# Kernel optimization log

Hardware: AMD Instinct MI355X
Metric: run time of the kernel (lower is better)

## Reference

```python
import jax, jax.numpy as jnp
import numpy as np

B, S, E, H, L, VL, VOCAB = 64, 256, 256, 256, 1024, 16, 50000


def setup_inputs() -> dict:
    key = jax.random.key(0)
    ks = jax.random.split(key, 16)
    n = lambda k, shape: jax.random.normal(k, shape, jnp.float32) * 0.05
    return {
        "x": jax.random.randint(ks[0], (B, S), 0, VOCAB),
        "V_idx": jax.random.randint(ks[1], (L, VL), 0, VOCAB),
        "emb": n(ks[2], (VOCAB, E)),
        "w_ih_f": n(ks[3], (3 * H, E)), "w_hh_f": n(ks[4], (3 * H, H)),
        "b_ih_f": n(ks[5], (3 * H,)), "b_hh_f": n(ks[6], (3 * H,)),
        "w_ih_b": n(ks[7], (3 * H, E)), "w_hh_b": n(ks[8], (3 * H, H)),
        "b_ih_b": n(ks[9], (3 * H,)), "b_hh_b": n(ks[10], (3 * H,)),
        "w1": n(ks[11], (E, 2 * H)), "b1": n(ks[12], (E,)),
        "w2": n(ks[13], (E, 2 * H)), "b2": n(ks[14], (E,)),
        "g1": jnp.ones((S,), jnp.float32), "be1": jnp.zeros((S,), jnp.float32),
        "g2": jnp.ones((L,), jnp.float32), "be2": jnp.zeros((L,), jnp.float32),
    }


def _gru_dir(xe, w_ih, w_hh, b_ih, b_hh, reverse):
    # xe: [B,S,E]; PyTorch GRU gate order: r, z, n
    Hh = w_hh.shape[1]
    gx = jnp.einsum('bse,ge->bsg', xe, w_ih) + b_ih      # [B,S,3H]
    gx = jnp.swapaxes(gx, 0, 1)                           # [S,B,3H]

    def step(h, g):
        gh = h @ w_hh.T + b_hh
        xr, xz, xn = jnp.split(g, 3, axis=-1)
        hr, hz, hn = jnp.split(gh, 3, axis=-1)
        r = jax.nn.sigmoid(xr + hr)
        z = jax.nn.sigmoid(xz + hz)
        nn = jnp.tanh(xn + r * hn)
        h_new = (1.0 - z) * nn + z * h
        return h_new, h_new

    h0 = jnp.zeros((xe.shape[0], Hh), xe.dtype)
    _, hs = jax.lax.scan(step, h0, gx, reverse=reverse)
    return jnp.swapaxes(hs, 0, 1)                         # [B,S,H]


def _bn(x, g, b):
    # BatchNorm1d training-mode over [B,C,F]: normalize over dims (0,2)
    m = x.mean(axis=(0, 2), keepdims=True)
    v = x.var(axis=(0, 2), keepdims=True)
    return g[None, :, None] * (x - m) * jax.lax.rsqrt(v + 1e-5) + b[None, :, None]


def reference(x, V_idx, emb, w_ih_f, w_hh_f, b_ih_f, b_hh_f,
              w_ih_b, w_hh_b, b_ih_b, b_hh_b,
              w1, b1, w2, b2, g1, be1, g2, be2):
    Vsum = emb[V_idx].sum(axis=1)                         # [L,E]
    xe = emb[x]                                           # [B,S,E]
    d = jnp.concatenate([
        _gru_dir(xe, w_ih_f, w_hh_f, b_ih_f, b_hh_f, False),
        _gru_dir(xe, w_ih_b, w_hh_b, b_ih_b, b_hh_b, True),
    ], axis=-1)                                           # [B,S,2H]
    d2 = jax.nn.relu(_bn(jnp.einsum('bsh,eh->bse', d, w1) + b1, g1, be1))  # [B,S,E]
    # fused version of the per-label python loop: tanh(d2 @ Vi) stacked over labels
    a = jnp.tanh(jnp.einsum('bse,le->bls', d2, Vsum))     # [B,L,S]
    c = jax.nn.relu(jnp.einsum('bls,bsh->blh', a, d))     # [B,L,2H]
    e = jnp.tanh(_bn(jnp.einsum('blh,eh->ble', c, w2) + b2, g2, be2))      # [B,L,E]
    eps = 1e-8
    num = jnp.sum(e * Vsum[None], axis=2)
    den = jnp.maximum(jnp.linalg.norm(e, axis=2), eps) * \
          jnp.maximum(jnp.linalg.norm(Vsum, axis=1)[None, :], eps)
    return num / den * 10.0                               # [B,L]
```

## Files before the change

kernel.cpp:

```cpp
#include <hip/hip_runtime.h>
#include <hip/hip_bf16.h>

#define Bz 64
#define Sz 256
#define Ez 256
#define Hz 256
#define Lz 1024
#define VLz 16

#define SCL 64.0f
#define DESCL (1.0f / 4096.0f)

typedef _Float16 half2_t __attribute__((ext_vector_type(2)));
typedef _Float16 half4_t __attribute__((ext_vector_type(4)));
typedef _Float16 f16x8   __attribute__((ext_vector_type(8)));
typedef float    f32x4   __attribute__((ext_vector_type(4)));

__device__ inline float fdot2(half2_t a, half2_t b, float c) {
#if __has_builtin(__builtin_amdgcn_fdot2)
    return __builtin_amdgcn_fdot2(a, b, c, false);
#else
    return c + (float)a[0] * (float)b[0] + (float)a[1] * (float)b[1];
#endif
}

__device__ inline void stage16(_Float16* ldst, const _Float16* gsrc) {
#if __has_builtin(__builtin_amdgcn_global_load_lds)
    __builtin_amdgcn_global_load_lds(
        (const __attribute__((address_space(1))) unsigned int*)gsrc,
        (__attribute__((address_space(3))) unsigned int*)ldst, 16, 0, 0);
#else
    *(f16x8*)ldst = *(const f16x8*)gsrc;
#endif
}

__global__ void vsum_kernel(const int* __restrict__ V_idx, const float* __restrict__ emb,
                            float* __restrict__ Vsum, _Float16* __restrict__ vsh,
                            _Float16* __restrict__ vsl, float* __restrict__ vnorm)
{
    int l = blockIdx.x, e = threadIdx.x;
    float s = 0.f;
#pragma unroll
    for (int j = 0; j < VLz; ++j) {
        int idx = V_idx[l * VLz + j];
        s += emb[(long)idx * Ez + e];
    }
    Vsum[l * Ez + e] = s;
    float t = s * SCL;
    _Float16 h = (_Float16)t;
    vsh[l * Ez + e] = h;
    vsl[l * Ez + e] = (_Float16)(t - (float)h);
    __shared__ float red[256];
    red[e] = s * s; __syncthreads();
    for (int off = 128; off > 0; off >>= 1) { if (e < off) red[e] += red[e + off]; __syncthreads(); }
    if (e == 0) vnorm[l] = sqrtf(red[0]);
}

__global__ void xe_kernel(const int* __restrict__ x, const float* __restrict__ emb,
                          _Float16* __restrict__ xeh, _Float16* __restrict__ xel)
{
    int i = blockIdx.x;
    int e = threadIdx.x;
    float v = emb[(long)x[i] * Ez + e] * SCL;
    _Float16 h = (_Float16)v;
    xeh[(long)i * Ez + e] = h;
    xel[(long)i * Ez + e] = (_Float16)(v - (float)h);
}

__global__ void wpack_kernel(const float* __restrict__ w_f, const float* __restrict__ w_b,
                             half2_t* __restrict__ out_f, half2_t* __restrict__ out_b)
{
    int i = blockIdx.x * 256 + threadIdx.x;
    int t = i & 255;
    int rest = i >> 8;
    int p = rest & 1;
    int gq = rest >> 1;
    int g = gq % 3;
    int kq = gq / 3;
    int o = g * 256 + t;
    int k = 4 * kq + 2 * p;
    out_f[i] = half2_t{(_Float16)w_f[o * 256 + k], (_Float16)w_f[o * 256 + k + 1]};
    out_b[i] = half2_t{(_Float16)w_b[o * 256 + k], (_Float16)w_b[o * 256 + k + 1]};
}

__global__ void cvtsplit_kernel(const float* __restrict__ in, _Float16* __restrict__ hi,
                                _Float16* __restrict__ lo, int n)
{
    int i = blockIdx.x * 256 + threadIdx.x;
    if (i < n) {
        float v = in[i] * SCL;
        _Float16 h = (_Float16)v;
        hi[i] = h;
        lo[i] = (_Float16)(v - (float)h);
    }
}

template<int EPI, int BIAS, int OUTM, int SPLIT_A>
__global__ __launch_bounds__(256, 2) void gemm_mfma(
    const _Float16* __restrict__ Ah, const _Float16* __restrict__ Al,
    const _Float16* __restrict__ Bh, const _Float16* __restrict__ Bl,
    const float* __restrict__ bias, const float* __restrict__ bias_b,
    float* __restrict__ C, _Float16* __restrict__ Ch, _Float16* __restrict__ Cl,
    int M, int N, int K, long sA, long sB, long sC)
{
    int bz = blockIdx.z;
    Ah += (long)bz * sA;
    if (SPLIT_A) Al += (long)bz * sA;
    Bh += (long)bz * sB;
    Bl += (long)bz * sB;
    const float* bp = BIAS ? (bz ? bias_b : bias) : nullptr;
    __shared__ __attribute__((aligned(16))) _Float16 Ash[128 * 32];
    __shared__ __attribute__((aligned(16))) _Float16 Asl[128 * 32];
    __shared__ __attribute__((aligned(16))) _Float16 Bsh[128 * 32];
    __shared__ __attribute__((aligned(16))) _Float16 Bsl[128 * 32];
    int tid = threadIdx.x;
    int lane = tid & 63;
    int wid = tid >> 6;
    int wm = wid >> 1, wn = wid & 1;
    int m0 = blockIdx.y * 128, n0 = blockIdx.x * 128;

    int srow = tid >> 2, sslot = tid & 3;
    int sw0 = sslot ^ ((srow >> 1) & 3);
    long a0 = (long)(m0 + srow) * K + sw0 * 8;
    long a1 = (long)(m0 + 64 + srow) * K + sw0 * 8;
    long b0 = (long)(n0 + srow) * K + sw0 * 8;
    long b1 = (long)(n0 + 64 + srow) * K + sw0 * 8;

    f32x4 acc[4][4] = {};
    int r16 = lane & 15, kg = lane >> 4;

    for (int k0 = 0; k0 < K; k0 += 32) {
        stage16(&Ash[tid * 8],        Ah + a0 + k0);
        stage16(&Ash[2048 + tid * 8], Ah + a1 + k0);
        if (SPLIT_A) {
            stage16(&Asl[tid * 8],        Al + a0 + k0);
            stage16(&Asl[2048 + tid * 8], Al + a1 + k0);
        }
        stage16(&Bsh[tid * 8],        Bh + b0 + k0);
        stage16(&Bsh[2048 + tid * 8], Bh + b1 + k0);
        stage16(&Bsl[tid * 8],        Bl + b0 + k0);
        stage16(&Bsl[2048 + tid * 8], Bl + b1 + k0);
        __syncthreads();
        f16x8 afh[4], afl[4], bfh[4], bfl[4];
#pragma unroll
        for (int mi = 0; mi < 4; ++mi) {
            int r = wm * 64 + mi * 16 + r16;
            int sl = kg ^ ((r >> 1) & 3);
            int off = r * 32 + sl * 8;
            afh[mi] = *(const f16x8*)&Ash[off];
            if (SPLIT_A) afl[mi] = *(const f16x8*)&Asl[off];
        }
#pragma unroll
        for (int ni = 0; ni < 4; ++ni) {
            int n = wn * 64 + ni * 16 + r16;
            int sl = kg ^ ((n >> 1) & 3);
            int off = n * 32 + sl * 8;
            bfh[ni] = *(const f16x8*)&Bsh[off];
            bfl[ni] = *(const f16x8*)&Bsl[off];
        }
#pragma unroll
        for (int mi = 0; mi < 4; ++mi)
#pragma unroll
            for (int ni = 0; ni < 4; ++ni) {
                acc[mi][ni] = __builtin_amdgcn_mfma_f32_16x16x32_f16(afh[mi], bfh[ni], acc[mi][ni], 0, 0, 0);
                acc[mi][ni] = __builtin_amdgcn_mfma_f32_16x16x32_f16(afh[mi], bfl[ni], acc[mi][ni], 0, 0, 0);
                if (SPLIT_A)
                    acc[mi][ni] = __builtin_amdgcn_mfma_f32_16x16x32_f16(afl[mi], bfh[ni], acc[mi][ni], 0, 0, 0);
            }
        __syncthreads();
    }

    long coff = (long)bz * sC;
#pragma unroll
    for (int mi = 0; mi < 4; ++mi) {
#pragma unroll
        for (int ni = 0; ni < 4; ++ni) {
            int n = n0 + wn * 64 + ni * 16 + r16;
            float bv = BIAS ? bp[n] : 0.f;
#pragma unroll
            for (int j = 0; j < 4; ++j) {
                int m = m0 + wm * 64 + mi * 16 + kg * 4 + j;
                float v = acc[mi][ni][j] * DESCL + bv;
                if (EPI == 1) v = fmaxf(v, 0.f);
                if (EPI == 2) v = tanhf(v);
                long idx = coff + (long)m * N + n;
                if (OUTM == 0) {
                    C[idx] = v;
                } else if (OUTM == 1) {
                    float t = v * SCL;
                    _Float16 h = (_Float16)t;
                    Ch[idx] = h;
                    Cl[idx] = (_Float16)(t - (float)h);
                } else {
                    Ch[idx] = (_Float16)(v * SCL);
                }
            }
        }
    }
}

__global__ __launch_bounds__(512, 2) void gru_kernel(
    const float* __restrict__ gx_f, const float* __restrict__ gx_b,
    const half2_t* __restrict__ wq_f, const half2_t* __restrict__ wq_b,
    const float* __restrict__ bhh_f, const float* __restrict__ bhh_b,
    _Float16* __restrict__ dh_out, _Float16* __restrict__ dl_out)
{
    int dir = blockIdx.x >> 6;
    int b   = blockIdx.x & 63;
    const float*   gx  = dir ? gx_b : gx_f;
    const half2_t* wq  = dir ? wq_b : wq_f;
    const float*   bhh = dir ? bhh_b : bhh_f;
    int tid = threadIdx.x;
    int t = tid & 255, q = tid >> 8;

    __shared__ __attribute__((aligned(16))) _Float16 hbuf[256];
    __shared__ float hf32[256];
    __shared__ float part[2 * 768];

    half2_t wr[192];
    const half2_t* wbase = wq + (size_t)q * 192 * 256 + t;
#pragma unroll
    for (int m = 0; m < 192; ++m) wr[m] = wbase[m << 8];

    float br = 0.f, bz = 0.f, bn = 0.f, hprev = 0.f;
    if (q == 0) {
        br = bhh[t]; bz = bhh[256 + t]; bn = bhh[512 + t];
        hbuf[t] = (_Float16)0.f;
        hf32[t] = 0.f;
    }
    __syncthreads();

    for (int step = 0; step < Sz; ++step) {
        int s = dir ? (Sz - 1 - step) : step;
        if (q == 1 && step > 0) {
            int sp = dir ? (Sz - step) : (step - 1);
            float hv = hf32[t] * SCL;
            _Float16 hh = (_Float16)hv;
            size_t idx = (size_t)(b * Sz + sp) * 512 + dir * 256 + t;
            dh_out[idx] = hh;
            dl_out[idx] = (_Float16)(hv - (float)hh);
        }
        const float* g = gx + (size_t)(b * Sz + s) * 768;
        float xr = 0.f, xz = 0.f, xn = 0.f;
        if (q == 0) { xr = g[t]; xz = g[256 + t]; xn = g[512 + t]; }

        float ar = 0.f, az = 0.f, an = 0.f;
        const half4_t* hp = (const half4_t*)hbuf;
#pragma unroll
        for (int jj = 0; jj < 32; ++jj) {
            half4_t hv = hp[q * 32 + jj];
            half2_t h01 = {hv[0], hv[1]};
            half2_t h23 = {hv[2], hv[3]};
            ar = fdot2(wr[jj * 6 + 0], h01, ar); ar = fdot2(wr[jj * 6 + 1], h23, ar);
            az = fdot2(wr[jj * 6 + 2], h01, az); az = fdot2(wr[jj * 6 + 3], h23, az);
            an = fdot2(wr[jj * 6 + 4], h01, an); an = fdot2(wr[jj * 6 + 5], h23, an);
        }
        part[q * 768 + t]       = ar;
        part[q * 768 + 256 + t] = az;
        part[q * 768 + 512 + t] = an;
        __syncthreads();

        if (q == 0) {
            float hr = part[t]       + part[768 + t];
            float hz = part[256 + t] + part[768 + 256 + t];
            float hn = part[512 + t] + part[768 + 512 + t];
            float r  = 1.f / (1.f + expf(-(xr + br + hr)));
            float z  = 1.f / (1.f + expf(-(xz + bz + hz)));
            float nn = tanhf(xn + r * (hn + bn));
            hprev = (1.f - z) * nn + z * hprev;
            hbuf[t] = (_Float16)hprev;
            hf32[t] = hprev;
        }
        __syncthreads();
    }
    if (q == 1) {
        int sl = dir ? 0 : (Sz - 1);
        float hv = hf32[t] * SCL;
        _Float16 hh = (_Float16)hv;
        size_t idx = (size_t)(b * Sz + sl) * 512 + dir * 256 + t;
        dh_out[idx] = hh;
        dl_out[idx] = (_Float16)(hv - (float)hh);
    }
}

__global__ __launch_bounds__(256) void dtrans_kernel(
    const _Float16* __restrict__ dh, const _Float16* __restrict__ dl,
    _Float16* __restrict__ dTh, _Float16* __restrict__ dTl)
{
    __shared__ _Float16 th[64][68];
    __shared__ _Float16 tl[64][68];
    int s0 = blockIdx.x << 6;
    int h0 = blockIdx.y << 6;
    int b  = blockIdx.z;
    int tid = threadIdx.x;
#pragma unroll
    for (int i = 0; i < 16; ++i) {
        int idx = tid + i * 256;
        int s = idx >> 6, h = idx & 63;
        size_t gi = (size_t)(b * 256 + s0 + s) * 512 + h0 + h;
        th[s][h] = dh[gi];
        tl[s][h] = dl[gi];
    }
    __syncthreads();
#pragma unroll
    for (int i = 0; i < 16; ++i) {
        int idx = tid + i * 256;
        int h = idx >> 6, s = idx & 63;
        size_t gi = (size_t)(b * 512 + h0 + h) * 256 + s0 + s;
        dTh[gi] = th[s][h];
        dTl[gi] = tl[s][h];
    }
}

__global__ void bn_stats_kernel(const float* __restrict__ y, int CH,
                                float* __restrict__ mean, float* __restrict__ istd)
{
    int c = blockIdx.x, t = threadIdx.x;
    float s = 0.f, ss = 0.f;
    for (int b = 0; b < Bz; ++b) {
        float v = y[((long)b * CH + c) * 256 + t];
        s += v; ss += v * v;
    }
    __shared__ float rs[256], rss[256];
    rs[t] = s; rss[t] = ss; __syncthreads();
    for (int off = 128; off > 0; off >>= 1) {
        if (t < off) { rs[t] += rs[t + off]; rss[t] += rss[t + off]; }
        __syncthreads();
    }
    if (t == 0) {
        float cnt = (float)(Bz * 256);
        float m = rs[0] / cnt;
        float var = rss[0] / cnt - m * m;
        mean[c] = m;
        istd[c] = rsqrtf(var + 1e-5f);
    }
}

__global__ void bn_apply_relu_kernel(const float* __restrict__ y,
                                     _Float16* __restrict__ yh, _Float16* __restrict__ yl,
                                     const float* __restrict__ mean, const float* __restrict__ istd,
                                     const float* __restrict__ g, const float* __restrict__ be)
{
    long i = (long)blockIdx.x * 256 + threadIdx.x;
    int c = (int)((i >> 8) % Sz);
    float v = (y[i] - mean[c]) * istd[c] * g[c] + be[c];
    v = fmaxf(v, 0.f);
    float t = v * SCL;
    _Float16 h = (_Float16)t;
    yh[i] = h;
    yl[i] = (_Float16)(t - (float)h);
}

__global__ void bn_tanh_out_kernel(const float* __restrict__ epre,
                                   const float* __restrict__ mean, const float* __restrict__ istd,
                                   const float* __restrict__ g, const float* __restrict__ be,
                                   const float* __restrict__ Vsum, const float* __restrict__ vnorm,
                                   float* __restrict__ out)
{
    int bl = blockIdx.x;
    int l = bl & (Lz - 1);
    int t = threadIdx.x;
    float v = (epre[(long)bl * 256 + t] - mean[l]) * istd[l] * g[l] + be[l];
    float ev = tanhf(v);
    float vv = Vsum[l * 256 + t];
    __shared__ float rd[256], rn[256];
    rd[t] = ev * vv; rn[t] = ev * ev; __syncthreads();
    for (int off = 128; off > 0; off >>= 1) {
        if (t < off) { rd[t] += rd[t + off]; rn[t] += rn[t + off]; }
        __syncthreads();
    }
    if (t == 0) {
        float num = rd[0];
        float den = fmaxf(sqrtf(rn[0]), 1e-8f) * fmaxf(vnorm[l], 1e-8f);
        out[bl] = num / den * 10.f;
    }
}

extern "C" void kernel_launch(void* const* d_in, const int* in_sizes, int n_in,
                              void* d_out, int out_size, void* d_ws, size_t ws_size,
                              hipStream_t stream)
{
    const int*   x      = (const int*)d_in[0];
    const int*   V_idx  = (const int*)d_in[1];
    const float* emb    = (const float*)d_in[2];
    const float* w_ih_f = (const float*)d_in[3];
    const float* w_hh_f = (const float*)d_in[4];
    const float* b_ih_f = (const float*)d_in[5];
    const float* b_hh_f = (const float*)d_in[6];
    const float* w_ih_b = (const float*)d_in[7];
    const float* w_hh_b = (const float*)d_in[8];
    const float* b_ih_b = (const float*)d_in[9];
    const float* b_hh_b = (const float*)d_in[10];
    const float* w1     = (const float*)d_in[11];
    const float* b1     = (const float*)d_in[12];
    const float* w2     = (const float*)d_in[13];
    const float* b2     = (const float*)d_in[14];
    const float* g1     = (const float*)d_in[15];
    const float* be1    = (const float*)d_in[16];
    const float* g2     = (const float*)d_in[17];
    const float* be2    = (const float*)d_in[18];

    float* ws = (float*)d_ws;
    float* out = (float*)d_out;

    float*    vsum   = ws;
    float*    vnorm  = ws + 262144;
    float*    mean   = ws + 263168;
    float*    istd   = ws + 264192;
    half2_t*  wqf    = (half2_t*)(ws + 265216);
    half2_t*  wqb    = (half2_t*)(ws + 363520);
    _Float16* vsh    = (_Float16*)(ws + 461824);
    _Float16* vsl    = (_Float16*)(ws + 592896);
    _Float16* wihh_f = (_Float16*)(ws + 723968);
    _Float16* wihl_f = (_Float16*)(ws + 822272);
    _Float16* wihh_b = (_Float16*)(ws + 920576);
    _Float16* wihl_b = (_Float16*)(ws + 1018880);
    _Float16* w1h    = (_Float16*)(ws + 1117184);
    _Float16* w1l    = (_Float16*)(ws + 1182720);
    _Float16* w2h    = (_Float16*)(ws + 1248256);
    _Float16* w2l    = (_Float16*)(ws + 1313792);
    float*    AB     = ws + 1379328;
    _Float16* xeh    = (_Float16*)(AB + 0);
    _Float16* xel    = (_Float16*)(AB + 2097152);
    float*    gxf    = AB + 4194304;
    float*    gxb    = AB + 16777216;
    _Float16* dh     = (_Float16*)(AB + 29360128);
    _Float16* dl     = (_Float16*)(AB + 33554432);
    _Float16* dTh    = (_Float16*)(AB + 0);
    _Float16* dTl    = (_Float16*)(AB + 4194304);
    float*    d2pre  = AB + 8388608;
    _Float16* d2h    = (_Float16*)(AB + 12582912);
    _Float16* d2l    = (_Float16*)(AB + 14680064);
    _Float16* ah     = (_Float16*)(AB + 16777216);
    _Float16* al     = (_Float16*)(AB + 25165824);
    _Float16* c16    = (_Float16*)(AB + 33554432);
    float*    epre   = AB + 0;

    vsum_kernel<<<Lz, 256, 0, stream>>>(V_idx, emb, vsum, vsh, vsl, vnorm);
    xe_kernel<<<Bz * Sz, 256, 0, stream>>>(x, emb, xeh, xel);
    wpack_kernel<<<384, 256, 0, stream>>>(w_hh_f, w_hh_b, wqf, wqb);
    cvtsplit_kernel<<<768, 256, 0, stream>>>(w_ih_f, wihh_f, wihl_f, 196608);
    cvtsplit_kernel<<<768, 256, 0, stream>>>(w_ih_b, wihh_b, wihl_b, 196608);
    cvtsplit_kernel<<<512, 256, 0, stream>>>(w1, w1h, w1l, 131072);
    cvtsplit_kernel<<<512, 256, 0, stream>>>(w2, w2h, w2l, 131072);

    gemm_mfma<0, 1, 0, 1><<<dim3(6, 128, 2), 256, 0, stream>>>(
        xeh, xel, wihh_f, wihl_f, b_ih_f, b_ih_b, gxf, nullptr, nullptr,
        Bz * Sz, 768, Ez, 0, 393216, 12582912);

    gru_kernel<<<128, 512, 0, stream>>>(gxf, gxb, wqf, wqb, b_hh_f, b_hh_b, dh, dl);
    dtrans_kernel<<<dim3(4, 8, Bz), 256, 0, stream>>>(dh, dl, dTh, dTl);

    gemm_mfma<0, 1, 0, 1><<<dim3(2, 128, 1), 256, 0, stream>>>(
        dh, dl, w1h, w1l, b1, b1, d2pre, nullptr, nullptr, Bz * Sz, Ez, 512, 0, 0, 0);
    bn_stats_kernel<<<Sz, 256, 0, stream>>>(d2pre, Sz, mean, istd);
    bn_apply_relu_kernel<<<Bz * Sz, 256, 0, stream>>>(d2pre, d2h, d2l, mean, istd, g1, be1);

    gemm_mfma<2, 0, 1, 1><<<dim3(2, 8, Bz), 256, 0, stream>>>(
        vsh, vsl, d2h, d2l, nullptr, nullptr, nullptr, ah, al,
        Lz, Sz, Ez, 0, (long)Sz * Ez, (long)Lz * Sz);

    gemm_mfma<1, 0, 2, 1><<<dim3(4, 8, Bz), 256, 0, stream>>>(
        ah, al, dTh, dTl, nullptr, nullptr, nullptr, c16, nullptr, Lz, 512, Sz,
        (long)Lz * Sz, (long)512 * Sz, (long)Lz * 512);

    gemm_mfma<0, 1, 0, 0><<<dim3(2, 512, 1), 256, 0, stream>>>(
        c16, nullptr, w2h, w2l, b2, b2, epre, nullptr, nullptr, Bz * Lz, Ez, 512, 0, 0, 0);
    bn_stats_kernel<<<Lz, 256, 0, stream>>>(epre, Lz, mean, istd);

    bn_tanh_out_kernel<<<Bz * Lz, 256, 0, stream>>>(epre, mean, istd, g2, be2, vsum, vnorm, out);
}
```

Measured before the change: 693.0 us.

## Process two batch rows per GRU block and stream recurrent weights from global

```diff
diff --git a/kernel.cpp b/kernel.cpp
--- a/kernel.cpp
+++ b/kernel.cpp
@@ -67,8 +67,8 @@
     xel[(long)i * Ez + e] = (_Float16)(v - (float)h);
 }
 
-__global__ void wpack_kernel(const float* __restrict__ w_f, const float* __restrict__ w_b,
-                             half2_t* __restrict__ out_f, half2_t* __restrict__ out_b)
+__global__ void wpack4_kernel(const float* __restrict__ w_f, const float* __restrict__ w_b,
+                              half2_t* __restrict__ out_f, half2_t* __restrict__ out_b)
 {
     int i = blockIdx.x * 256 + threadIdx.x;
     int t = i & 255;
@@ -79,8 +79,12 @@
     int kq = gq / 3;
     int o = g * 256 + t;
     int k = 4 * kq + 2 * p;
-    out_f[i] = half2_t{(_Float16)w_f[o * 256 + k], (_Float16)w_f[o * 256 + k + 1]};
-    out_b[i] = half2_t{(_Float16)w_b[o * 256 + k], (_Float16)w_b[o * 256 + k + 1]};
+    int q  = rest / 192;
+    int m  = rest % 192;
+    int ch = m >> 2, pos = m & 3;
+    int ni = ((q * 48 + ch) * 256 + t) * 4 + pos;
+    out_f[ni] = half2_t{(_Float16)w_f[o * 256 + k], (_Float16)w_f[o * 256 + k + 1]};
+    out_b[ni] = half2_t{(_Float16)w_b[o * 256 + k], (_Float16)w_b[o * 256 + k + 1]};
 }
 
 __global__ void cvtsplit_kernel(const float* __restrict__ in, _Float16* __restrict__ hi,
@@ -201,86 +205,111 @@
 
 __global__ __launch_bounds__(512, 2) void gru_kernel(
     const float* __restrict__ gx_f, const float* __restrict__ gx_b,
-    const half2_t* __restrict__ wq_f, const half2_t* __restrict__ wq_b,
+    const f16x8* __restrict__ wq4_f, const f16x8* __restrict__ wq4_b,
     const float* __restrict__ bhh_f, const float* __restrict__ bhh_b,
     _Float16* __restrict__ dh_out, _Float16* __restrict__ dl_out)
 {
-    int dir = blockIdx.x >> 6;
-    int b   = blockIdx.x & 63;
-    const float*   gx  = dir ? gx_b : gx_f;
-    const half2_t* wq  = dir ? wq_b : wq_f;
-    const float*   bhh = dir ? bhh_b : bhh_f;
+    int dir = blockIdx.x >> 5;
+    int b0  = (blockIdx.x & 31) * 2;
+    const float* gx  = dir ? gx_b : gx_f;
+    const f16x8* wq4 = dir ? wq4_b : wq4_f;
+    const float* bhh = dir ? bhh_b : bhh_f;
     int tid = threadIdx.x;
     int t = tid & 255, q = tid >> 8;
 
-    __shared__ __attribute__((aligned(16))) _Float16 hbuf[256];
-    __shared__ float hf32[256];
-    __shared__ float part[2 * 768];
-
-    half2_t wr[192];
-    const half2_t* wbase = wq + (size_t)q * 192 * 256 + t;
-#pragma unroll
-    for (int m = 0; m < 192; ++m) wr[m] = wbase[m << 8];
-
-    float br = 0.f, bz = 0.f, bn = 0.f, hprev = 0.f;
-    if (q == 0) {
-        br = bhh[t]; bz = bhh[256 + t]; bn = bhh[512 + t];
-        hbuf[t] = (_Float16)0.f;
-        hf32[t] = 0.f;
-    }
+    __shared__ __attribute__((aligned(16))) _Float16 hbuf[2][256];
+    __shared__ float part[12 * 256];
+#define PART(beta, qq, g) (((((beta) * 2 + (qq)) * 3 + (g)) << 8))
+
+    const f16x8* w4 = wq4 + (size_t)q * 48 * 256 + t;
+
+    float br = bhh[t], bz = bhh[256 + t], bn = bhh[512 + t];
+    float hprev = 0.f;
+    if (q == 0) { hbuf[0][t] = (_Float16)0.f; hbuf[1][t] = (_Float16)0.f; }
     __syncthreads();
 
     for (int step = 0; step < Sz; ++step) {
         int s = dir ? (Sz - 1 - step) : step;
-        if (q == 1 && step > 0) {
+        if (step > 0) {
             int sp = dir ? (Sz - step) : (step - 1);
-            float hv = hf32[t] * SCL;
+            float hv = hprev * SCL;
             _Float16 hh = (_Float16)hv;
-            size_t idx = (size_t)(b * Sz + sp) * 512 + dir * 256 + t;
+            size_t idx = (size_t)((b0 + q) * Sz + sp) * 512 + dir * 256 + t;
             dh_out[idx] = hh;
             dl_out[idx] = (_Float16)(hv - (float)hh);
         }
-        const float* g = gx + (size_t)(b * Sz + s) * 768;
-        float xr = 0.f, xz = 0.f, xn = 0.f;
-        if (q == 0) { xr = g[t]; xz = g[256 + t]; xn = g[512 + t]; }
-
-        float ar = 0.f, az = 0.f, an = 0.f;
-        const half4_t* hp = (const half4_t*)hbuf;
-#pragma unroll
-        for (int jj = 0; jj < 32; ++jj) {
-            half4_t hv = hp[q * 32 + jj];
-            half2_t h01 = {hv[0], hv[1]};
-            half2_t h23 = {hv[2], hv[3]};
-            ar = fdot2(wr[jj * 6 + 0], h01, ar); ar = fdot2(wr[jj * 6 + 1], h23, ar);
-            az = fdot2(wr[jj * 6 + 2], h01, az); az = fdot2(wr[jj * 6 + 3], h23, az);
-            an = fdot2(wr[jj * 6 + 4], h01, an); an = fdot2(wr[jj * 6 + 5], h23, an);
-        }
-        part[q * 768 + t]       = ar;
-        part[q * 768 + 256 + t] = az;
-        part[q * 768 + 512 + t] = an;
+        const float* g = gx + (size_t)((b0 + q) * Sz + s) * 768;
+        float xr = g[t], xz = g[256 + t], xn = g[512 + t];
+
+        float ar0 = 0.f, az0 = 0.f, an0 = 0.f;
+        float ar1 = 0.f, az1 = 0.f, an1 = 0.f;
+        const half4_t* h0q = (const half4_t*)hbuf[0] + q * 32;
+        const half4_t* h1q = (const half4_t*)hbuf[1] + q * 32;
+#pragma unroll
+        for (int cj = 0; cj < 16; ++cj) {
+            f16x8 c0 = w4[(3 * cj + 0) * 256];
+            f16x8 c1 = w4[(3 * cj + 1) * 256];
+            f16x8 c2 = w4[(3 * cj + 2) * 256];
+            half4_t ha0 = h0q[2 * cj], hb0 = h0q[2 * cj + 1];
+            half4_t ha1 = h1q[2 * cj], hb1 = h1q[2 * cj + 1];
+            half2_t a01_0 = {ha0[0], ha0[1]}, a23_0 = {ha0[2], ha0[3]};
+            half2_t b01_0 = {hb0[0], hb0[1]}, b23_0 = {hb0[2], hb0[3]};
+            half2_t a01_1 = {ha1[0], ha1[1]}, a23_1 = {ha1[2], ha1[3]};
+            half2_t b01_1 = {hb1[0], hb1[1]}, b23_1 = {hb1[2], hb1[3]};
+            ar0 = fdot2(half2_t{c0[0], c0[1]}, a01_0, ar0);
+            ar0 = fdot2(half2_t{c0[2], c0[3]}, a23_0, ar0);
+            az0 = fdot2(half2_t{c0[4], c0[5]}, a01_0, az0);
+            az0 = fdot2(half2_t{c0[6], c0[7]}, a23_0, az0);
+            an0 = fdot2(half2_t{c1[0], c1[1]}, a01_0, an0);
+            an0 = fdot2(half2_t{c1[2], c1[3]}, a23_0, an0);
+            ar0 = fdot2(half2_t{c1[4], c1[5]}, b01_0, ar0);
+            ar0 = fdot2(half2_t{c1[6], c1[7]}, b23_0, ar0);
+            az0 = fdot2(half2_t{c2[0], c2[1]}, b01_0, az0);
+            az0 = fdot2(half2_t{c2[2], c2[3]}, b23_0, az0);
+            an0 = fdot2(half2_t{c2[4], c2[5]}, b01_0, an0);
+            an0 = fdot2(half2_t{c2[6], c2[7]}, b23_0, an0);
+            ar1 = fdot2(half2_t{c0[0], c0[1]}, a01_1, ar1);
+            ar1 = fdot2(half2_t{c0[2], c0[3]}, a23_1, ar1);
+            az1 = fdot2(half2_t{c0[4], c0[5]}, a01_1, az1);
+            az1 = fdot2(half2_t{c0[6], c0[7]}, a23_1, az1);
+            an1 = fdot2(half2_t{c1[0], c1[1]}, a01_1, an1);
+            an1 = fdot2(half2_t{c1[2], c1[3]}, a23_1, an1);
+            ar1 = fdot2(half2_t{c1[4], c1[5]}, b01_1, ar1);
+            ar1 = fdot2(half2_t{c1[6], c1[7]}, b23_1, ar1);
+            az1 = fdot2(half2_t{c2[0], c2[1]}, b01_1, az1);
+            az1 = fdot2(half2_t{c2[2], c2[3]}, b23_1, az1);
+            an1 = fdot2(half2_t{c2[4], c2[5]}, b01_1, an1);
+            an1 = fdot2(half2_t{c2[6], c2[7]}, b23_1, an1);
+        }
+        part[PART(0, q, 0) + t] = ar0;
+        part[PART(0, q, 1) + t] = az0;
+        part[PART(0, q, 2) + t] = an0;
+        part[PART(1, q, 0) + t] = ar1;
+        part[PART(1, q, 1) + t] = az1;
+        part[PART(1, q, 2) + t] = an1;
         __syncthreads();
 
-        if (q == 0) {
-            float hr = part[t]       + part[768 + t];
-            float hz = part[256 + t] + part[768 + 256 + t];
-            float hn = part[512 + t] + part[768 + 512 + t];
+        {
+            float hr = part[PART(q, 0, 0) + t] + part[PART(q, 1, 0) + t];
+            float hz = part[PART(q, 0, 1) + t] + part[PART(q, 1, 1) + t];
+            float hn = part[PART(q, 0, 2) + t] + part[PART(q, 1, 2) + t];
             float r  = 1.f / (1.f + expf(-(xr + br + hr)));
             float z  = 1.f / (1.f + expf(-(xz + bz + hz)));
             float nn = tanhf(xn + r * (hn + bn));
             hprev = (1.f - z) * nn + z * hprev;
-            hbuf[t] = (_Float16)hprev;
-            hf32[t] = hprev;
+            hbuf[q][t] = (_Float16)hprev;
         }
         __syncthreads();
     }
-    if (q == 1) {
+    {
         int sl = dir ? 0 : (Sz - 1);
-        float hv = hf32[t] * SCL;
+        float hv = hprev * SCL;
         _Float16 hh = (_Float16)hv;
-        size_t idx = (size_t)(b * Sz + sl) * 512 + dir * 256 + t;
+        size_t idx = (size_t)((b0 + q) * Sz + sl) * 512 + dir * 256 + t;
         dh_out[idx] = hh;
         dl_out[idx] = (_Float16)(hv - (float)hh);
     }
+#undef PART
 }
 
 __global__ __launch_bounds__(256) void dtrans_kernel(
@@ -438,7 +467,7 @@
 
     vsum_kernel<<<Lz, 256, 0, stream>>>(V_idx, emb, vsum, vsh, vsl, vnorm);
     xe_kernel<<<Bz * Sz, 256, 0, stream>>>(x, emb, xeh, xel);
-    wpack_kernel<<<384, 256, 0, stream>>>(w_hh_f, w_hh_b, wqf, wqb);
+    wpack4_kernel<<<384, 256, 0, stream>>>(w_hh_f, w_hh_b, wqf, wqb);
     cvtsplit_kernel<<<768, 256, 0, stream>>>(w_ih_f, wihh_f, wihl_f, 196608);
     cvtsplit_kernel<<<768, 256, 0, stream>>>(w_ih_b, wihh_b, wihl_b, 196608);
     cvtsplit_kernel<<<512, 256, 0, stream>>>(w1, w1h, w1l, 131072);
@@ -448,7 +477,8 @@
         xeh, xel, wihh_f, wihl_f, b_ih_f, b_ih_b, gxf, nullptr, nullptr,
         Bz * Sz, 768, Ez, 0, 393216, 12582912);
 
-    gru_kernel<<<128, 512, 0, stream>>>(gxf, gxb, wqf, wqb, b_hh_f, b_hh_b, dh, dl);
+    gru_kernel<<<64, 512, 0, stream>>>(gxf, gxb, (const f16x8*)wqf, (const f16x8*)wqb,
+                                       b_hh_f, b_hh_b, dh, dl);
     dtrans_kernel<<<dim3(4, 8, Bz), 256, 0, stream>>>(dh, dl, dTh, dTl);
 
     gemm_mfma<0, 1, 0, 1><<<dim3(2, 128, 1), 256, 0, stream>>>(
```

Result: slower. 890.1 us (+28.4%).
